# Performance work log

Hardware: AMD Instinct MI355X
Metric: run time of the kernel (lower is better)

The kernel has to match this reference:

```python
import jax, jax.numpy as jnp
from jax import lax
import numpy as np

BATCH = 524288
SEQ_LEN = 64


def setup_inputs() -> dict:
    key = jax.random.key(0)
    ka, kb = jax.random.split(key)
    a = jax.random.randint(ka, (BATCH, SEQ_LEN), 0, 10).astype(jnp.float32)
    b = jax.random.randint(kb, (BATCH, SEQ_LEN), 0, 10).astype(jnp.float32)
    # RNNCell params as hardcoded in Adder._initialize_weights
    weight_ih = jnp.array([[1.0, 1.0]], dtype=jnp.float32)   # (hidden=1, input=2)
    weight_hh = jnp.array([[1.0]], dtype=jnp.float32)        # (1, 1)
    bias_ih = jnp.zeros((1,), dtype=jnp.float32)
    bias_hh = jnp.zeros((1,), dtype=jnp.float32)
    return {"a": a, "b": b, "weight_ih": weight_ih, "weight_hh": weight_hh,
            "bias_ih": bias_ih, "bias_hh": bias_hh}


def reference(a, b, weight_ih, weight_hh, bias_ih, bias_hh):
    # a, b: (B, S) base-10 digits; carry h: (B, 1) hidden state.
    # Process digits from least significant (rightmost) to most significant.
    xs = jnp.stack([a, b], axis=-1)            # (B, S, 2)
    xs = jnp.flip(xs, axis=1)                  # reversed digit order
    xs = jnp.swapaxes(xs, 0, 1)                # (S, B, 2) for scan

    def step(h, x):
        # RNNCell with relu: u = relu(x @ W_ih^T + b_ih + h @ W_hh^T + b_hh)
        u = jax.nn.relu(x @ weight_ih.T + bias_ih + h @ weight_hh.T + bias_hh)  # (B,1)
        carry = jax.nn.relu(u - 9.0) - jax.nn.relu(u - 10.0)                    # (B,1)
        s = x[:, 0] + x[:, 1] + h[:, 0]                                         # (B,)
        digit = s - 10.0 * carry[:, 0]                                          # (B,)
        return carry, digit

    h0 = jnp.zeros((a.shape[0], 1), dtype=a.dtype)
    _, digits_rev = lax.scan(step, h0, xs)     # (S, B), least-significant first
    digits = jnp.flip(digits_rev, axis=0).T    # (B, S), original order
    return digits
```

## Files before the change

### kernel.cpp

```cpp
#include <hip/hip_runtime.h>


__global__ __launch_bounds__(256) void adder_kernel(
    const float* __restrict__ a,
    const float* __restrict__ b,
    float* __restrict__ out,
    long long n_rows)
{
    const int lane = (int)(threadIdx.x & 63);
    const long long row = (long long)blockIdx.x * 4 + (threadIdx.x >> 6);
    if (row >= n_rows) return;

    const long long idx = row * 64 + lane;
    const float s = a[idx] + b[idx];

    const unsigned long long g_l = __ballot(s >= 10.0f);
    const unsigned long long p_l = __ballot(s == 9.0f);

    const unsigned long long G  = __brevll(g_l);
    const unsigned long long P  = __brevll(p_l);
    const unsigned long long PG = P | G;
    const unsigned long long C_pos = (PG + G) ^ PG ^ G;
    const unsigned long long C_l   = __brevll(C_pos);

    const float cin = (float)((C_l >> lane) & 1ULL);
    const float u = s + cin;
    const float carry_out = (u >= 10.0f) ? 1.0f : 0.0f;
    out[idx] = u - 10.0f * carry_out;
}

extern "C" void kernel_launch(void* const* d_in, const int* in_sizes, int n_in,
                              void* d_out, int out_size, void* d_ws, size_t ws_size,
                              hipStream_t stream) {
    const float* a = (const float*)d_in[0];
    const float* b = (const float*)d_in[1];
    float* out = (float*)d_out;

    const long long n_rows = (long long)in_sizes[0] / 64;
    const int blocks = (int)((n_rows + 3) / 4);
    adder_kernel<<<blocks, 256, 0, stream>>>(a, b, out, n_rows);
}
```

Before: 307.8 us.

## Vectorize digit adder with float4 per lane and grid-stride persistent waves

Each lane now loads four digits as a float4, so one wave handles four rows. Carry handling becomes two levels: a serial ripple over the four digits inside a lane, then a 16-bit ballot carry-lookahead across the lanes of each row. The launch is capped at 2048 blocks, each looping over rows with a grid stride. The aim is wider memory transactions and fewer blocks for this memory-bound kernel, at the cost of more per-lane serial ALU work and a limited number of blocks in flight.

```diff
diff --git a/kernel.cpp b/kernel.cpp
--- a/kernel.cpp
+++ b/kernel.cpp
@@ -2,41 +2,74 @@
 
 
 __global__ __launch_bounds__(256) void adder_kernel(
-    const float* __restrict__ a,
-    const float* __restrict__ b,
-    float* __restrict__ out,
+    const float4* __restrict__ a,
+    const float4* __restrict__ b,
+    float4* __restrict__ out,
     long long n_rows)
 {
     const int lane = (int)(threadIdx.x & 63);
-    const long long row = (long long)blockIdx.x * 4 + (threadIdx.x >> 6);
-    if (row >= n_rows) return;
+    const int k    = lane >> 4;
+    const int blk  = lane & 15;
+    const int pos  = 15 - blk;
 
-    const long long idx = row * 64 + lane;
-    const float s = a[idx] + b[idx];
+    const long long wave_id     = (long long)blockIdx.x * 4 + (threadIdx.x >> 6);
+    const long long wave_stride = (long long)gridDim.x * 4;
+    const long long n_wave_work = (n_rows + 3) >> 2;
 
-    const unsigned long long g_l = __ballot(s >= 10.0f);
-    const unsigned long long p_l = __ballot(s == 9.0f);
+    for (long long w = wave_id; w < n_wave_work; w += wave_stride) {
+        const long long row = w * 4 + k;
+        const bool ok = row < n_rows;
+        const long long v4 = (ok ? row : 0) * 16 + blk;
 
-    const unsigned long long G  = __brevll(g_l);
-    const unsigned long long P  = __brevll(p_l);
-    const unsigned long long PG = P | G;
-    const unsigned long long C_pos = (PG + G) ^ PG ^ G;
-    const unsigned long long C_l   = __brevll(C_pos);
+        const float4 av = a[v4];
+        const float4 bv = b[v4];
+        const float s0 = av.x + bv.x;
+        const float s1 = av.y + bv.y;
+        const float s2 = av.z + bv.z;
+        const float s3 = av.w + bv.w;
 
-    const float cin = (float)((C_l >> lane) & 1ULL);
-    const float u = s + cin;
-    const float carry_out = (u >= 10.0f) ? 1.0f : 0.0f;
-    out[idx] = u - 10.0f * carry_out;
+        float gc = (s3 >= 10.0f) ? 1.0f : 0.0f;
+        gc = (s2 + gc >= 10.0f) ? 1.0f : 0.0f;
+        gc = (s1 + gc >= 10.0f) ? 1.0f : 0.0f;
+        gc = (s0 + gc >= 10.0f) ? 1.0f : 0.0f;
+        const bool Gb = (gc != 0.0f);
+        const bool Pb = (s0 == 9.0f) && (s1 == 9.0f) &&
+                        (s2 == 9.0f) && (s3 == 9.0f);
+
+        const unsigned long long g_mask = __ballot(Gb);
+        const unsigned long long p_mask = __ballot(Pb);
+        unsigned int g16 = (unsigned int)(g_mask >> (k * 16)) & 0xFFFFu;
+        unsigned int p16 = (unsigned int)(p_mask >> (k * 16)) & 0xFFFFu;
+        g16 = __brev(g16) >> 16;
+        p16 = __brev(p16) >> 16;
+        const unsigned int pg  = p16 | g16;
+        const unsigned int c16 = (pg + g16) ^ pg ^ g16;
+        const float cin = (float)((c16 >> pos) & 1u);
+
+        const float u3 = s3 + cin; const float c3 = (u3 >= 10.0f) ? 1.0f : 0.0f;
+        const float u2 = s2 + c3;  const float c2 = (u2 >= 10.0f) ? 1.0f : 0.0f;
+        const float u1 = s1 + c2;  const float c1 = (u1 >= 10.0f) ? 1.0f : 0.0f;
+        const float u0 = s0 + c1;  const float c0 = (u0 >= 10.0f) ? 1.0f : 0.0f;
+
+        float4 dv;
+        dv.x = u0 - 10.0f * c0;
+        dv.y = u1 - 10.0f * c1;
+        dv.z = u2 - 10.0f * c2;
+        dv.w = u3 - 10.0f * c3;
+        if (ok) out[v4] = dv;
+    }
 }
 
 extern "C" void kernel_launch(void* const* d_in, const int* in_sizes, int n_in,
                               void* d_out, int out_size, void* d_ws, size_t ws_size,
                               hipStream_t stream) {
-    const float* a = (const float*)d_in[0];
-    const float* b = (const float*)d_in[1];
-    float* out = (float*)d_out;
+    const float4* a = (const float4*)d_in[0];
+    const float4* b = (const float4*)d_in[1];
+    float4* out = (float4*)d_out;
 
-    const long long n_rows = (long long)in_sizes[0] / 64;
-    const int blocks = (int)((n_rows + 3) / 4);
-    adder_kernel<<<blocks, 256, 0, stream>>>(a, b, out, n_rows);
+    const long long n_rows  = (long long)in_sizes[0] / 64;
+    const long long n_waves = (n_rows + 3) / 4;
+    long long blocks = (n_waves + 3) / 4;
+    if (blocks > 2048) blocks = 2048;
+    adder_kernel<<<(int)blocks, 256, 0, stream>>>(a, b, out, n_rows);
 }
```

New measurement: 318.3 us. 1.03x slower.
